# Kernel optimization log

Measured on AMD Instinct MI355X. Metric: run time of the kernel, lower is better.

The kernel has to match this reference:

```python
import jax, jax.numpy as jnp
import numpy as np
from jax import lax

SINKHORN_ITERS = 20
SINKHORN_REG = 0.05
OT_BLUR = 0.05
OT_ITERS = 20
LAMBDA_OT = 0.1
LAMBDA_REG = 0.01
N_SUB = 2048


def pairwise_dist_sq(a, b):
    # a: [B,N,3], b: [B,M,3] -> [B,N,M]
    a_sq = jnp.sum(a * a, axis=-1, keepdims=True)          # [B,N,1]
    b_sq = jnp.sum(b * b, axis=-1, keepdims=True)          # [B,M,1]
    ab = jnp.einsum('bnd,bmd->bnm', a, b)
    return jnp.maximum(a_sq + jnp.swapaxes(b_sq, 1, 2) - 2.0 * ab, 0.0)


def farthest_point_sample(x, n_sub):
    # x: [B,N,3] -> int32 indices [B,n_sub]; sequential min-distance update loop
    B, N, _ = x.shape

    def body(i, state):
        dists, farthest, sel = state
        sel = sel.at[:, i].set(farthest)
        centroid = jnp.take_along_axis(x, farthest[:, None, None], axis=1)  # [B,1,3]
        d = jnp.sum((x - centroid) ** 2, axis=-1)                            # [B,N]
        dists = jnp.minimum(dists, d)
        farthest = jnp.argmax(dists, axis=-1).astype(jnp.int32)
        return dists, farthest, sel

    dists = jnp.full((B, N), jnp.inf, dtype=x.dtype)
    farthest = jnp.zeros((B,), dtype=jnp.int32)
    sel = jnp.zeros((B, n_sub), dtype=jnp.int32)
    _, _, sel = lax.fori_loop(0, n_sub, body, (dists, farthest, sel))
    return sel


def sinkhorn_assignment(cost, n_iters=SINKHORN_ITERS, reg=SINKHORN_REG):
    # log-domain Sinkhorn -> soft doubly-stochastic P [B,N,M]
    log_K = -cost / reg
    B, N, M = cost.shape
    log_u = jnp.zeros((B, N), dtype=cost.dtype)
    log_v = jnp.zeros((B, M), dtype=cost.dtype)

    def body(carry, _):
        lu, lv = carry
        lu = -jax.nn.logsumexp(log_K + lv[:, None, :], axis=2)
        lv = -jax.nn.logsumexp(log_K + lu[:, :, None], axis=1)
        return (lu, lv), None

    (log_u, log_v), _ = lax.scan(body, (log_u, log_v), None, length=n_iters)
    return jnp.exp(log_K + log_u[:, :, None] + log_v[:, None, :])


def _ot_eps(x, y, eps, n_iters=OT_ITERS):
    # balanced entropic OT dual value per batch (geomloss sinkhorn, p=2: C=|x-y|^2/2)
    C = 0.5 * pairwise_dist_sq(x, y)
    B, N, M = C.shape
    log_mu = -jnp.log(jnp.asarray(N, C.dtype))
    log_nu = -jnp.log(jnp.asarray(M, C.dtype))
    f = jnp.zeros((B, N), dtype=C.dtype)
    g = jnp.zeros((B, M), dtype=C.dtype)

    def body(carry, _):
        f, g = carry
        f = -eps * jax.nn.logsumexp((g[:, None, :] - C) / eps + log_nu, axis=2)
        g = -eps * jax.nn.logsumexp((f[:, :, None] - C) / eps + log_mu, axis=1)
        return (f, g), None

    (f, g), _ = lax.scan(body, (f, g), None, length=n_iters)
    return jnp.mean(f, axis=1) + jnp.mean(g, axis=1)  # [B]


def sinkhorn_divergence(x, y, eps):
    return jnp.mean(_ot_eps(x, y, eps) - 0.5 * _ot_eps(x, x, eps) - 0.5 * _ot_eps(y, y, eps))


def _forward(target_sub, idx_dummy, t, template, W_enc, b_enc, W1, b1, W2, b2):
    pass


def setup_inputs() -> dict:
    key = jax.random.key(0)
    ks = jax.random.split(key, 9)
    B, N = 8, 16384
    d_z, d_h = 256, 256
    return {
        'target': jax.random.normal(ks[0], (B, N, 3), dtype=jnp.float32),
        't': jax.random.uniform(ks[1], (B,), dtype=jnp.float32),
        'template': jax.random.normal(ks[2], (N_SUB, 3), dtype=jnp.float32),
        'W_enc': jax.random.normal(ks[3], (3, d_z), dtype=jnp.float32) * 0.05,
        'b_enc': jnp.zeros((d_z,), dtype=jnp.float32),
        'W1': jax.random.normal(ks[4], (3 + 1 + d_z, d_h), dtype=jnp.float32) * 0.05,
        'b1': jnp.zeros((d_h,), dtype=jnp.float32),
        'W2': jax.random.normal(ks[5], (d_h, 3), dtype=jnp.float32) * 0.05,
        'b2': jnp.zeros((3,), dtype=jnp.float32),
    }


def reference(target, t, template, W_enc, b_enc, W1, b1, W2, b2):
    B, N, _ = target.shape
    n_sub = template.shape[0]
    t = jnp.clip(t, 1e-5, 1.0 - 1e-5)

    # FPS subsample target (n_sub < N); template already at n_sub points
    idx = farthest_point_sample(target, n_sub)                        # [B,n_sub]
    target_sub = jnp.take_along_axis(target, idx[:, :, None], axis=1)  # [B,n_sub,3]
    template_sub = jnp.broadcast_to(template[None], (B, n_sub, 3))

    # Sinkhorn OT alignment
    cost = pairwise_dist_sq(template_sub, target_sub)                  # [B,n_sub,n_sub]
    P = sinkhorn_assignment(cost)
    target_perm = jnp.einsum('bnm,bmd->bnd', P, target_sub)

    # straight-line interpolant + gt velocity
    v_gt = target_perm - template_sub
    t_ = t[:, None, None]
    x_t = (1.0 - t_) * template_sub + t_ * target_perm

    # encode (stand-in model): per-point linear + max-pool
    feat = jax.nn.relu(target_sub @ W_enc + b_enc)                     # [B,n_sub,d_z]
    z = jnp.max(feat, axis=1)                                          # [B,d_z]

    # velocity prediction (stand-in MLP conditioned on x_t, t, z)
    h_in = jnp.concatenate([
        x_t,
        jnp.broadcast_to(t_, (B, n_sub, 1)),
        jnp.broadcast_to(z[:, None, :], (B, n_sub, z.shape[-1])),
    ], axis=-1)
    v_pred = jax.nn.relu(h_in @ W1 + b1) @ W2 + b2                      # [B,n_sub,3]

    loss_velocity = jnp.mean((v_pred - v_gt) ** 2)

    # OT loss on x1 approx (no grad through v_pred, matching torch.no_grad)
    x_1_approx = template_sub + lax.stop_gradient(v_pred)
    eps = jnp.asarray(OT_BLUR ** 2, target.dtype)
    loss_ot = sinkhorn_divergence(x_1_approx, target_sub, eps)

    # template regularisation towards unit norm
    template_norms = jnp.sqrt(jnp.sum(template * template, axis=-1))
    loss_reg = jnp.mean((template_norms - 1.0) ** 2)

    loss = loss_velocity + LAMBDA_OT * loss_ot + LAMBDA_REG * loss_reg
    return loss, loss_velocity, loss_ot, loss_reg
```

## Files before the change

### kernel.cpp

```cpp
#include <hip/hip_runtime.h>
#include <math.h>

#define NPTS 16384
#define NB 8
#define NS 2048
#define DZ 256

typedef float v2f __attribute__((ext_vector_type(2)));

#define OFF_SCAL 0
#define OFF_LU   64
#define OFF_LV   (OFF_LU + NB*NS)
#define OFF_F    (OFF_LV + NB*NS)
#define OFF_G    (OFF_F + 3*NB*NS)
#define ZERO_FLOATS (OFF_G + 3*NB*NS)
#define OFF_IDX  ZERO_FLOATS
#define OFF_YP   (OFF_IDX + NB*NS)
#define OFF_TP   (OFF_YP + NB*NS*4)
#define OFF_XP   (OFF_TP + NS*4)
#define OFF_PERM (OFF_XP + NB*NS*4)
#define OFF_Z    (OFF_PERM + NB*NS*3)
#define OFF_HB   (OFF_Z + NB*DZ)

__global__ __launch_bounds__(512) void fps_kernel(const float* __restrict__ x,
                                                  int* __restrict__ sel){
  #pragma clang fp contract(off)
  const int b = blockIdx.x, tid = threadIdx.x;
  const float* xb = x + (size_t)b * NPTS * 3;
  float c[96];
  {
    const float4* s4 = (const float4*)(xb + (size_t)tid * 96);
    #pragma unroll
    for (int q = 0; q < 24; q++){
      float4 v = s4[q];
      c[4*q] = v.x; c[4*q+1] = v.y; c[4*q+2] = v.z; c[4*q+3] = v.w;
    }
  }
  v2f X[16], Y[16], Z[16], D[16];
  #pragma unroll
  for (int j = 0; j < 16; j++){
    X[j] = (v2f){c[6*j],   c[6*j+3]};
    Y[j] = (v2f){c[6*j+1], c[6*j+4]};
    Z[j] = (v2f){c[6*j+2], c[6*j+5]};
    D[j] = (v2f){INFINITY, INFINITY};
  }
  __shared__ unsigned long long sK[2][8];
  float c0 = xb[0], c1 = xb[1], c2 = xb[2];
  int widx = 0;
  const int wv = tid >> 6, lane = tid & 63;

  for (int i = 0; i < NS; i++){
    if (tid == 0) sel[b*NS + i] = widx;
    const v2f c0v = {c0,c0}, c1v = {c1,c1}, c2v = {c2,c2};
    #pragma unroll
    for (int j = 0; j < 16; j++){
      v2f dx = X[j] - c0v;
      v2f dy = Y[j] - c1v;
      v2f dz = Z[j] - c2v;
      v2f d2 = (dx*dx + dy*dy) + dz*dz;
      D[j] = __builtin_elementwise_min(D[j], d2);
    }
    v2f m0 = __builtin_elementwise_max(D[0],  D[1]);
    v2f m1 = __builtin_elementwise_max(D[2],  D[3]);
    v2f m2 = __builtin_elementwise_max(D[4],  D[5]);
    v2f m3 = __builtin_elementwise_max(D[6],  D[7]);
    v2f m4 = __builtin_elementwise_max(D[8],  D[9]);
    v2f m5 = __builtin_elementwise_max(D[10], D[11]);
    v2f m6 = __builtin_elementwise_max(D[12], D[13]);
    v2f m7 = __builtin_elementwise_max(D[14], D[15]);
    m0 = __builtin_elementwise_max(m0, m1);
    m2 = __builtin_elementwise_max(m2, m3);
    m4 = __builtin_elementwise_max(m4, m5);
    m6 = __builtin_elementwise_max(m6, m7);
    m0 = __builtin_elementwise_max(m0, m2);
    m4 = __builtin_elementwise_max(m4, m6);
    m0 = __builtin_elementwise_max(m0, m4);
    const float lmax = fmaxf(m0.x, m0.y);
    int kk = 31;
    #pragma unroll
    for (int j = 15; j >= 0; j--){
      if (D[j].y == lmax) kk = 2*j + 1;
      if (D[j].x == lmax) kk = 2*j;
    }
    unsigned long long key =
      ((unsigned long long)(~__float_as_uint(lmax)) << 32) |
      (unsigned int)(tid*32 + kk);
    #pragma unroll
    for (int o = 32; o; o >>= 1){
      unsigned long long ok = __shfl_xor(key, o, 64);
      key = (ok < key) ? ok : key;
    }
    const int par = i & 1;
    if (lane == 0) sK[par][wv] = key;
    __syncthreads();
    unsigned long long best = sK[par][0];
    #pragma unroll
    for (int w = 1; w < 8; w++){
      unsigned long long k2 = sK[par][w];
      best = (k2 < best) ? k2 : best;
    }
    widx = (int)(best & 0xffffffffu);
    const float* cp = xb + (size_t)widx * 3;
    c0 = cp[0]; c1 = cp[1]; c2 = cp[2];
  }
}

__global__ __launch_bounds__(256) void gather_pack_kernel(const float* __restrict__ x,
                                                          const int* __restrict__ sel,
                                                          float4* __restrict__ yp){
  const int b = blockIdx.y;
  const int k = blockIdx.x*256 + threadIdx.x;
  const int p = sel[b*NS + k];
  const float* s = x + ((size_t)b*NPTS + p)*3;
  const float x0 = s[0], x1 = s[1], x2 = s[2];
  const float sq = fmaf(x0,x0, fmaf(x1,x1, x2*x2));
  yp[b*NS + k] = make_float4(x0, x1, x2, sq);
}

__global__ __launch_bounds__(256) void pack_t_kernel(const float* __restrict__ tmpl,
                                                     float4* __restrict__ tp,
                                                     float* __restrict__ sumreg){
  __shared__ float sbuf[4];
  const int k = blockIdx.x*256 + threadIdx.x;
  const float x0 = tmpl[3*k], x1 = tmpl[3*k+1], x2 = tmpl[3*k+2];
  const float sq = fmaf(x0,x0, fmaf(x1,x1, x2*x2));
  tp[k] = make_float4(x0, x1, x2, sq);
  const float n = sqrtf(sq) - 1.0f;
  float v = n*n;
  #pragma unroll
  for (int o = 32; o; o >>= 1) v += __shfl_xor(v, o, 64);
  if ((threadIdx.x & 63) == 0) sbuf[threadIdx.x >> 6] = v;
  __syncthreads();
  if (threadIdx.x == 0){
    float t = 0.f;
    for (int w = 0; w < 4; w++) t += sbuf[w];
    atomicAdd(sumreg, t);
  }
}

__global__ __launch_bounds__(256) void feat_z_kernel(const float4* __restrict__ yp,
                                                     const float* __restrict__ Wenc,
                                                     const float* __restrict__ benc,
                                                     float* __restrict__ z){
  __shared__ float4 sy[NS];
  const int b = blockIdx.x, tid = threadIdx.x;
  for (int j = tid; j < NS; j += 256) sy[j] = yp[b*NS + j];
  __syncthreads();
  const float w0 = Wenc[tid], w1 = Wenc[256+tid], w2 = Wenc[512+tid], bb = benc[tid];
  float m = -INFINITY;
  for (int n = 0; n < NS; n++){
    float4 q = sy[n];
    float v = fmaf(q.x, w0, fmaf(q.y, w1, fmaf(q.z, w2, bb)));
    m = fmaxf(m, fmaxf(v, 0.0f));
  }
  z[b*DZ + tid] = m;
}

__global__ __launch_bounds__(256) void hbase_kernel(const float* __restrict__ z,
                                                    const float* __restrict__ W1,
                                                    const float* __restrict__ b1,
                                                    const float* __restrict__ tarr,
                                                    float* __restrict__ hb){
  __shared__ float sz[DZ];
  const int b = blockIdx.x, cidx = threadIdx.x;
  sz[cidx] = z[b*DZ + cidx];
  __syncthreads();
  const float t = fminf(fmaxf(tarr[b], 1e-5f), (float)(1.0 - 1e-5));
  float acc = fmaf(t, W1[3*256 + cidx], b1[cidx]);
  for (int k = 0; k < DZ; k++) acc = fmaf(sz[k], W1[(4 + k)*256 + cidx], acc);
  hb[b*DZ + cidx] = acc;
}

__device__ __forceinline__ void sink_pass_core(const float4* __restrict__ PI, long piStride,
                                               const float4* __restrict__ PJ, long pjStride,
                                               const float* __restrict__ dIn,
                                               float* __restrict__ dOut,
                                               float H, float twoH, float dMul, float dAdd,
                                               float oScale, float4* S){
  const int tid = threadIdx.x;
  const int b = blockIdx.z;
  {
    const float4* pj = PJ + pjStride*b;
    const float* din = dIn + (size_t)b*NS;
    for (int j = tid; j < NS; j += 1024){
      float4 q = pj[j];
      float E = fmaf(-H, q.w, fmaf(din[j], dMul, dAdd));
      S[j] = make_float4(q.x, q.y, q.z, E);
    }
  }
  __syncthreads();
  const int w = tid >> 6, lane = tid & 63;
  const int i = blockIdx.x*16 + w;
  const float4 pi = PI[piStride*b + i];
  const float R = -H*pi.w;
  float mx = -INFINITY, s = 0.0f;
  #pragma unroll 2
  for (int k = 0; k < 8; k++){
    const int j0 = k*256 + lane;
    float4 a0 = S[j0], a1 = S[j0+64], a2 = S[j0+128], a3 = S[j0+192];
    float v0 = fmaf(twoH, fmaf(pi.x,a0.x, fmaf(pi.y,a0.y, pi.z*a0.z)), a0.w + R);
    float v1 = fmaf(twoH, fmaf(pi.x,a1.x, fmaf(pi.y,a1.y, pi.z*a1.z)), a1.w + R);
    float v2 = fmaf(twoH, fmaf(pi.x,a2.x, fmaf(pi.y,a2.y, pi.z*a2.z)), a2.w + R);
    float v3 = fmaf(twoH, fmaf(pi.x,a3.x, fmaf(pi.y,a3.y, pi.z*a3.z)), a3.w + R);
    float m4 = fmaxf(fmaxf(v0, v1), fmaxf(v2, v3));
    float nm = fmaxf(mx, m4);
    s = fmaf(s, __expf(mx - nm),
             __expf(v0 - nm) + __expf(v1 - nm) + __expf(v2 - nm) + __expf(v3 - nm));
    mx = nm;
  }
  #pragma unroll
  for (int o = 32; o; o >>= 1){
    float om = __shfl_xor(mx, o, 64);
    float os = __shfl_xor(s,  o, 64);
    float nm = fmaxf(mx, om);
    s = fmaf(s, __expf(mx - nm), os*__expf(om - nm));
    mx = nm;
  }
  if (lane == 0) dOut[(size_t)b*NS + i] = oScale*(mx + __logf(s));
}

__global__ __launch_bounds__(1024) void sink_assign_kernel(const float4* __restrict__ tp,
                                                           const float4* __restrict__ yp,
                                                           float* __restrict__ lu,
                                                           float* __restrict__ lv,
                                                           int dir, float H, float twoH){
  __shared__ float4 S[NS];
  if (dir == 0) sink_pass_core(tp, 0,  yp, NS, lv, lu, H, twoH, 1.0f, 0.0f, -1.0f, S);
  else          sink_pass_core(yp, NS, tp, 0,  lu, lv, H, twoH, 1.0f, 0.0f, -1.0f, S);
}

__global__ __launch_bounds__(1024) void sink_ot_kernel(const float4* __restrict__ xp,
                                                       const float4* __restrict__ yp,
                                                       float* __restrict__ F,
                                                       float* __restrict__ G,
                                                       int dir, float H, float twoH,
                                                       float dMul, float dAdd, float oScale){
  __shared__ float4 S[NS];
  const int p = blockIdx.y;
  const float4* first  = (p == 2) ? yp : xp;
  const float4* second = (p == 1) ? xp : yp;
  float* f = F + (size_t)p*NB*NS;
  float* g = G + (size_t)p*NB*NS;
  if (dir == 0) sink_pass_core(first,  NS, second, NS, g, f, H, twoH, dMul, dAdd, oScale, S);
  else          sink_pass_core(second, NS, first,  NS, f, g, H, twoH, dMul, dAdd, oScale, S);
}

__global__ __launch_bounds__(1024) void perm_kernel(const float4* __restrict__ tp,
                                                    const float4* __restrict__ yp,
                                                    const float* __restrict__ lu,
                                                    const float* __restrict__ lv,
                                                    float* __restrict__ perm,
                                                    float H, float twoH){
  __shared__ float4 S[NS];
  const int tid = threadIdx.x, b = blockIdx.z;
  for (int j = tid; j < NS; j += 1024){
    float4 q = yp[(size_t)b*NS + j];
    float E = fmaf(-H, q.w, lv[(size_t)b*NS + j]);
    S[j] = make_float4(q.x, q.y, q.z, E);
  }
  __syncthreads();
  const int w = tid >> 6, lane = tid & 63;
  const int i = blockIdx.x*16 + w;
  const float4 pi = tp[i];
  const float R = fmaf(-H, pi.w, lu[(size_t)b*NS + i]);
  float a0 = 0.f, a1 = 0.f, a2 = 0.f;
  #pragma unroll 2
  for (int k = 0; k < 8; k++){
    #pragma unroll
    for (int u = 0; u < 4; u++){
      const int j = k*256 + u*64 + lane;
      float4 q = S[j];
      float val = fmaf(twoH, fmaf(pi.x,q.x, fmaf(pi.y,q.y, pi.z*q.z)), q.w + R);
      float wgt = __expf(val);
      a0 = fmaf(wgt, q.x, a0);
      a1 = fmaf(wgt, q.y, a1);
      a2 = fmaf(wgt, q.z, a2);
    }
  }
  #pragma unroll
  for (int o = 32; o; o >>= 1){
    a0 += __shfl_xor(a0, o, 64);
    a1 += __shfl_xor(a1, o, 64);
    a2 += __shfl_xor(a2, o, 64);
  }
  if (lane == 0){
    float* d = perm + ((size_t)b*NS + i)*3;
    d[0] = a0; d[1] = a1; d[2] = a2;
  }
}

__global__ __launch_bounds__(128) void mlp_kernel(const float4* __restrict__ tp,
                                                  const float* __restrict__ perm,
                                                  const float* __restrict__ hb,
                                                  const float* __restrict__ W1,
                                                  const float* __restrict__ W2,
                                                  const float* __restrict__ b2,
                                                  const float* __restrict__ tarr,
                                                  float4* __restrict__ xp,
                                                  float* __restrict__ sumvel){
  __shared__ float sw0[256], sw1[256], sw2[256], shb[256], sW2[768];
  __shared__ float sred[2];
  const int tid = threadIdx.x;
  const int r = blockIdx.x*128 + tid;
  const int b = r >> 11, n = r & (NS - 1);
  for (int k = tid; k < 256; k += 128){
    sw0[k] = W1[k]; sw1[k] = W1[256+k]; sw2[k] = W1[512+k]; shb[k] = hb[b*256 + k];
  }
  for (int k = tid; k < 768; k += 128) sW2[k] = W2[k];
  __syncthreads();
  const float t = fminf(fmaxf(tarr[b], 1e-5f), (float)(1.0 - 1e-5));
  const float4 T = tp[n];
  const float pm0 = perm[(size_t)r*3], pm1 = perm[(size_t)r*3+1], pm2 = perm[(size_t)r*3+2];
  const float omt = 1.0f - t;
  const float xt0 = omt*T.x + t*pm0;
  const float xt1 = omt*T.y + t*pm1;
  const float xt2 = omt*T.z + t*pm2;
  float a0 = b2[0], a1 = b2[1], a2 = b2[2];
  for (int cc = 0; cc < 256; cc++){
    float pre = fmaf(xt0, sw0[cc], fmaf(xt1, sw1[cc], fmaf(xt2, sw2[cc], shb[cc])));
    float h = fmaxf(pre, 0.0f);
    a0 = fmaf(h, sW2[3*cc],   a0);
    a1 = fmaf(h, sW2[3*cc+1], a1);
    a2 = fmaf(h, sW2[3*cc+2], a2);
  }
  const float vg0 = pm0 - T.x, vg1 = pm1 - T.y, vg2 = pm2 - T.z;
  const float d0 = a0 - vg0, d1 = a1 - vg1, d2 = a2 - vg2;
  float ls = fmaf(d0,d0, fmaf(d1,d1, d2*d2));
  const float x0 = T.x + a0, x1 = T.y + a1, x2 = T.z + a2;
  const float sq = fmaf(x0,x0, fmaf(x1,x1, x2*x2));
  xp[r] = make_float4(x0, x1, x2, sq);
  #pragma unroll
  for (int o = 32; o; o >>= 1) ls += __shfl_xor(ls, o, 64);
  if ((tid & 63) == 0) sred[tid >> 6] = ls;
  __syncthreads();
  if (tid == 0) atomicAdd(sumvel, sred[0] + sred[1]);
}

__global__ __launch_bounds__(256) void ot_sum_kernel(const float* __restrict__ F,
                                                     const float* __restrict__ G,
                                                     float* __restrict__ ot){
  __shared__ float sbuf[8];
  const int pb = blockIdx.x;
  const float* f = F + (size_t)pb*NS;
  const float* g = G + (size_t)pb*NS;
  float sf = 0.f, sg = 0.f;
  for (int j = threadIdx.x; j < NS; j += 256){ sf += f[j]; sg += g[j]; }
  #pragma unroll
  for (int o = 32; o; o >>= 1){ sf += __shfl_xor(sf, o, 64); sg += __shfl_xor(sg, o, 64); }
  if ((threadIdx.x & 63) == 0){ sbuf[threadIdx.x >> 6] = sf; sbuf[4 + (threadIdx.x >> 6)] = sg; }
  __syncthreads();
  if (threadIdx.x == 0){
    float tf = 0.f, tg = 0.f;
    for (int w = 0; w < 4; w++){ tf += sbuf[w]; tg += sbuf[4 + w]; }
    ot[pb] = tf/(float)NS + tg/(float)NS;
  }
}

__global__ void finalize_kernel(const float* __restrict__ scal, float* __restrict__ out){
  if (threadIdx.x == 0){
    const float* ot = scal + 2;
    float lot = 0.f;
    for (int b = 0; b < NB; b++)
      lot += ot[0*NB + b] - 0.5f*ot[1*NB + b] - 0.5f*ot[2*NB + b];
    lot /= (float)NB;
    const float lvv = scal[0] / (float)(NB*NS*3);
    const float lrg = scal[1] / (float)NS;
    out[0] = lvv + 0.1f*lot + 0.01f*lrg;
    out[1] = lvv;
    out[2] = lot;
    out[3] = lrg;
  }
}

extern "C" void kernel_launch(void* const* d_in, const int* in_sizes, int n_in,
                              void* d_out, int out_size, void* d_ws, size_t ws_size,
                              hipStream_t stream){
  (void)in_sizes; (void)n_in; (void)out_size; (void)ws_size;
  const float* target = (const float*)d_in[0];
  const float* tarr   = (const float*)d_in[1];
  const float* tmpl   = (const float*)d_in[2];
  const float* Wenc   = (const float*)d_in[3];
  const float* benc   = (const float*)d_in[4];
  const float* W1     = (const float*)d_in[5];
  const float* b1     = (const float*)d_in[6];
  const float* W2     = (const float*)d_in[7];
  const float* b2     = (const float*)d_in[8];
  float* out = (float*)d_out;
  float* ws  = (float*)d_ws;

  float*  scal = ws + OFF_SCAL;
  float*  lu   = ws + OFF_LU;
  float*  lv   = ws + OFF_LV;
  float*  F    = ws + OFF_F;
  float*  G    = ws + OFF_G;
  int*    sel  = (int*)(ws + OFF_IDX);
  float4* yp   = (float4*)(ws + OFF_YP);
  float4* tp   = (float4*)(ws + OFF_TP);
  float4* xp   = (float4*)(ws + OFF_XP);
  float*  perm = ws + OFF_PERM;
  float*  z    = ws + OFF_Z;
  float*  hb   = ws + OFF_HB;

  hipMemsetAsync(ws, 0, (size_t)ZERO_FLOATS*sizeof(float), stream);

  fps_kernel<<<NB, 512, 0, stream>>>(target, sel);
  gather_pack_kernel<<<dim3(8, NB), 256, 0, stream>>>(target, sel, yp);
  pack_t_kernel<<<8, 256, 0, stream>>>(tmpl, tp, scal + 1);
  feat_z_kernel<<<NB, 256, 0, stream>>>(yp, Wenc, benc, z);
  hbase_kernel<<<NB, 256, 0, stream>>>(z, W1, b1, tarr, hb);

  const float INVREG = 1.0f/0.05f;
  for (int it = 0; it < 20; ++it){
    sink_assign_kernel<<<dim3(128,1,NB), 1024, 0, stream>>>(tp, yp, lu, lv, 0, INVREG, 2.0f*INVREG);
    sink_assign_kernel<<<dim3(128,1,NB), 1024, 0, stream>>>(tp, yp, lu, lv, 1, INVREG, 2.0f*INVREG);
  }
  perm_kernel<<<dim3(128,1,NB), 1024, 0, stream>>>(tp, yp, lu, lv, perm, INVREG, 2.0f*INVREG);
  mlp_kernel<<<128, 128, 0, stream>>>(tp, perm, hb, W1, W2, b2, tarr, xp, scal + 0);

  const float EPS    = (float)(0.05*0.05);
  const float INVEPS = 1.0f/EPS;
  const float HOT    = 0.5f*INVEPS;
  const float LOGNU  = (float)(-log(2048.0));
  for (int it = 0; it < 20; ++it){
    sink_ot_kernel<<<dim3(128,3,NB), 1024, 0, stream>>>(xp, yp, F, G, 0, HOT, INVEPS, INVEPS, LOGNU, -EPS);
    sink_ot_kernel<<<dim3(128,3,NB), 1024, 0, stream>>>(xp, yp, F, G, 1, HOT, INVEPS, INVEPS, LOGNU, -EPS);
  }
  ot_sum_kernel<<<24, 256, 0, stream>>>(F, G, scal + 2);
  finalize_kernel<<<1, 64, 0, stream>>>(scal, out);
}
```

Baseline: 5.748 ms.

## Restructure FPS argmax reduction: float-max shuffle, ballot, and winner-thread broadcast

The per-iteration argmax in farthest point sampling now reduces a plain float max with shuffles and picks the first matching lane by ballot, instead of shuffling 64-bit keys. Only the winning thread locates its local index and writes the centroid coordinates to shared memory, so the dependent global load of the next centroid is removed. This adds a second __syncthreads per iteration and drops the double-buffered key array. Launch bounds now request two blocks per CU.

```diff
diff --git a/kernel.cpp b/kernel.cpp
--- a/kernel.cpp
+++ b/kernel.cpp
@@ -22,8 +22,8 @@
 #define OFF_Z    (OFF_PERM + NB*NS*3)
 #define OFF_HB   (OFF_Z + NB*DZ)
 
-__global__ __launch_bounds__(512) void fps_kernel(const float* __restrict__ x,
-                                                  int* __restrict__ sel){
+__global__ __launch_bounds__(512, 2) void fps_kernel(const float* __restrict__ x,
+                                                     int* __restrict__ sel){
   #pragma clang fp contract(off)
   const int b = blockIdx.x, tid = threadIdx.x;
   const float* xb = x + (size_t)b * NPTS * 3;
@@ -44,7 +44,9 @@
     Z[j] = (v2f){c[6*j+2], c[6*j+5]};
     D[j] = (v2f){INFINITY, INFINITY};
   }
-  __shared__ unsigned long long sK[2][8];
+  __shared__ unsigned long long sK[8];
+  __shared__ float sC[3];
+  __shared__ int sW;
   float c0 = xb[0], c1 = xb[1], c2 = xb[2];
   int widx = 0;
   const int wv = tid >> 6, lane = tid & 63;
@@ -76,32 +78,37 @@
     m4 = __builtin_elementwise_max(m4, m6);
     m0 = __builtin_elementwise_max(m0, m4);
     const float lmax = fmaxf(m0.x, m0.y);
-    int kk = 31;
+    float wmax = lmax;
     #pragma unroll
-    for (int j = 15; j >= 0; j--){
-      if (D[j].y == lmax) kk = 2*j + 1;
-      if (D[j].x == lmax) kk = 2*j;
-    }
-    unsigned long long key =
-      ((unsigned long long)(~__float_as_uint(lmax)) << 32) |
-      (unsigned int)(tid*32 + kk);
-    #pragma unroll
-    for (int o = 32; o; o >>= 1){
-      unsigned long long ok = __shfl_xor(key, o, 64);
-      key = (ok < key) ? ok : key;
-    }
-    const int par = i & 1;
-    if (lane == 0) sK[par][wv] = key;
+    for (int o = 32; o; o >>= 1) wmax = fmaxf(wmax, __shfl_xor(wmax, o, 64));
+    const unsigned long long bal = __ballot(lmax == wmax);
+    if (lane == 0){
+      const int ftid = wv*64 + (__ffsll(bal) - 1);
+      sK[wv] = ((unsigned long long)(~__float_as_uint(wmax)) << 32) | (unsigned)ftid;
+    }
     __syncthreads();
-    unsigned long long best = sK[par][0];
+    unsigned long long best = sK[0];
     #pragma unroll
     for (int w = 1; w < 8; w++){
-      unsigned long long k2 = sK[par][w];
+      unsigned long long k2 = sK[w];
       best = (k2 < best) ? k2 : best;
     }
-    widx = (int)(best & 0xffffffffu);
-    const float* cp = xb + (size_t)widx * 3;
-    c0 = cp[0]; c1 = cp[1]; c2 = cp[2];
+    const int wtid = (int)(best & 0xffffffffu);
+    if (tid == wtid){
+      const float bmax = __uint_as_float(~(unsigned)(best >> 32));
+      int kk = 31;
+      float px = 0.f, py = 0.f, pz = 0.f;
+      #pragma unroll
+      for (int j = 15; j >= 0; j--){
+        if (D[j].y == bmax){ kk = 2*j + 1; px = X[j].y; py = Y[j].y; pz = Z[j].y; }
+        if (D[j].x == bmax){ kk = 2*j;     px = X[j].x; py = Y[j].x; pz = Z[j].x; }
+      }
+      sW = tid*32 + kk;
+      sC[0] = px; sC[1] = py; sC[2] = pz;
+    }
+    __syncthreads();
+    widx = sW;
+    c0 = sC[0]; c1 = sC[1]; c2 = sC[2];
   }
 }
 
```

After: 5.933 ms. 1.03x slower.

## Restructure FPS argmax with DPP wave max, ballot, and shared centroid broadcast

Applied to the files above, without the earlier changes.

Restructures the per-iteration argmax in the farthest point sampling loop. The running max is folded into the distance update, a DPP-based wave max replaces the 64-bit key shuffle reduction, and ballot picks the first winning lane. Only that lane computes the index and writes the centroid coordinates to shared memory. This drops the dependent global load of the new centroid from the serial loop, shortening the critical path per iteration, at the cost of extra shared traffic and a launch-bounds occupancy hint.

```diff
diff --git a/kernel.cpp b/kernel.cpp
--- a/kernel.cpp
+++ b/kernel.cpp
@@ -22,8 +22,25 @@
 #define OFF_Z    (OFF_PERM + NB*NS*3)
 #define OFF_HB   (OFF_Z + NB*DZ)
 
-__global__ __launch_bounds__(512) void fps_kernel(const float* __restrict__ x,
-                                                  int* __restrict__ sel){
+__device__ __forceinline__ float wave_max_dpp(float v){
+  int t;
+  t = __builtin_amdgcn_update_dpp(__float_as_int(v), __float_as_int(v), 0x111, 0xf, 0xf, false);
+  v = fmaxf(v, __int_as_float(t));
+  t = __builtin_amdgcn_update_dpp(__float_as_int(v), __float_as_int(v), 0x112, 0xf, 0xf, false);
+  v = fmaxf(v, __int_as_float(t));
+  t = __builtin_amdgcn_update_dpp(__float_as_int(v), __float_as_int(v), 0x114, 0xf, 0xf, false);
+  v = fmaxf(v, __int_as_float(t));
+  t = __builtin_amdgcn_update_dpp(__float_as_int(v), __float_as_int(v), 0x118, 0xf, 0xf, false);
+  v = fmaxf(v, __int_as_float(t));
+  t = __builtin_amdgcn_update_dpp(__float_as_int(v), __float_as_int(v), 0x142, 0xa, 0xf, false);
+  v = fmaxf(v, __int_as_float(t));
+  t = __builtin_amdgcn_update_dpp(__float_as_int(v), __float_as_int(v), 0x143, 0xc, 0xf, false);
+  v = fmaxf(v, __int_as_float(t));
+  return __shfl(v, 63, 64);
+}
+
+__global__ __launch_bounds__(512, 2) void fps_kernel(const float* __restrict__ x,
+                                                     int* __restrict__ sel){
   #pragma clang fp contract(off)
   const int b = blockIdx.x, tid = threadIdx.x;
   const float* xb = x + (size_t)b * NPTS * 3;
@@ -45,63 +62,54 @@
     D[j] = (v2f){INFINITY, INFINITY};
   }
   __shared__ unsigned long long sK[2][8];
+  __shared__ float4 sC[2][8];
   float c0 = xb[0], c1 = xb[1], c2 = xb[2];
   int widx = 0;
   const int wv = tid >> 6, lane = tid & 63;
 
   for (int i = 0; i < NS; i++){
     if (tid == 0) sel[b*NS + i] = widx;
-    const v2f c0v = {c0,c0}, c1v = {c1,c1}, c2v = {c2,c2};
+    const float n0 = -c0, n1 = -c1, n2 = -c2;
+    const v2f n0v = {n0,n0}, n1v = {n1,n1}, n2v = {n2,n2};
+    v2f lm = {0.0f, 0.0f};
     #pragma unroll
     for (int j = 0; j < 16; j++){
-      v2f dx = X[j] - c0v;
-      v2f dy = Y[j] - c1v;
-      v2f dz = Z[j] - c2v;
+      v2f dx = X[j] + n0v;
+      v2f dy = Y[j] + n1v;
+      v2f dz = Z[j] + n2v;
       v2f d2 = (dx*dx + dy*dy) + dz*dz;
-      D[j] = __builtin_elementwise_min(D[j], d2);
-    }
-    v2f m0 = __builtin_elementwise_max(D[0],  D[1]);
-    v2f m1 = __builtin_elementwise_max(D[2],  D[3]);
-    v2f m2 = __builtin_elementwise_max(D[4],  D[5]);
-    v2f m3 = __builtin_elementwise_max(D[6],  D[7]);
-    v2f m4 = __builtin_elementwise_max(D[8],  D[9]);
-    v2f m5 = __builtin_elementwise_max(D[10], D[11]);
-    v2f m6 = __builtin_elementwise_max(D[12], D[13]);
-    v2f m7 = __builtin_elementwise_max(D[14], D[15]);
-    m0 = __builtin_elementwise_max(m0, m1);
-    m2 = __builtin_elementwise_max(m2, m3);
-    m4 = __builtin_elementwise_max(m4, m5);
-    m6 = __builtin_elementwise_max(m6, m7);
-    m0 = __builtin_elementwise_max(m0, m2);
-    m4 = __builtin_elementwise_max(m4, m6);
-    m0 = __builtin_elementwise_max(m0, m4);
-    const float lmax = fmaxf(m0.x, m0.y);
-    int kk = 31;
-    #pragma unroll
-    for (int j = 15; j >= 0; j--){
-      if (D[j].y == lmax) kk = 2*j + 1;
-      if (D[j].x == lmax) kk = 2*j;
-    }
-    unsigned long long key =
-      ((unsigned long long)(~__float_as_uint(lmax)) << 32) |
-      (unsigned int)(tid*32 + kk);
-    #pragma unroll
-    for (int o = 32; o; o >>= 1){
-      unsigned long long ok = __shfl_xor(key, o, 64);
-      key = (ok < key) ? ok : key;
-    }
+      v2f nd = __builtin_elementwise_min(D[j], d2);
+      D[j] = nd;
+      lm = __builtin_elementwise_max(lm, nd);
+    }
+    const float lmax = fmaxf(lm.x, lm.y);
+    const float wmax = wave_max_dpp(lmax);
+    const unsigned long long bal = __ballot(lmax == wmax);
+    const int ftid = wv*64 + (__ffsll((long long)bal) - 1);
     const int par = i & 1;
-    if (lane == 0) sK[par][wv] = key;
+    if (tid == ftid){
+      int kk = 31;
+      float px = 0.f, py = 0.f, pz = 0.f;
+      #pragma unroll
+      for (int j = 15; j >= 0; j--){
+        if (D[j].y == wmax){ kk = 2*j + 1; px = X[j].y; py = Y[j].y; pz = Z[j].y; }
+        if (D[j].x == wmax){ kk = 2*j;     px = X[j].x; py = Y[j].x; pz = Z[j].x; }
+      }
+      sK[par][wv] = ((unsigned long long)(~__float_as_uint(wmax)) << 32) |
+                    (unsigned)(tid*32 + kk);
+      sC[par][wv] = make_float4(px, py, pz, 0.f);
+    }
     __syncthreads();
     unsigned long long best = sK[par][0];
+    int sidx = 0;
     #pragma unroll
     for (int w = 1; w < 8; w++){
       unsigned long long k2 = sK[par][w];
-      best = (k2 < best) ? k2 : best;
+      if (k2 < best){ best = k2; sidx = w; }
     }
     widx = (int)(best & 0xffffffffu);
-    const float* cp = xb + (size_t)widx * 3;
-    c0 = cp[0]; c1 = cp[1]; c2 = cp[2];
+    const float4 cc = sC[par][sidx];
+    c0 = cc.x; c1 = cc.y; c2 = cc.z;
   }
 }
 
```

Result: slower. 7.822 ms (+36.1%).

## Process four rows per wave in Sinkhorn passes to reuse shared tiles

Applied to the files above, without the earlier changes.

Each wavefront now computes the logsumexp for four output rows instead of one, reusing every shared-memory column load across the four rows. The grid is shrunk accordingly from 128 to 32 blocks per batch, which also cuts the redundant per-block staging of the column data into shared memory. The trade-offs are higher register pressure and fewer blocks, which lowers occupancy and latency hiding.

```diff
diff --git a/kernel.cpp b/kernel.cpp
--- a/kernel.cpp
+++ b/kernel.cpp
@@ -190,33 +190,46 @@
   }
   __syncthreads();
   const int w = tid >> 6, lane = tid & 63;
-  const int i = blockIdx.x*16 + w;
-  const float4 pi = PI[piStride*b + i];
-  const float R = -H*pi.w;
-  float mx = -INFINITY, s = 0.0f;
+  const int i0 = blockIdx.x*64 + w*4;
+  float4 pi[4];
+  float  R[4], mx[4], ss[4];
+  #pragma unroll
+  for (int r = 0; r < 4; r++){
+    pi[r] = PI[piStride*b + i0 + r];
+    R[r]  = -H*pi[r].w;
+    mx[r] = -INFINITY;
+    ss[r] = 0.0f;
+  }
   #pragma unroll 2
   for (int k = 0; k < 8; k++){
     const int j0 = k*256 + lane;
     float4 a0 = S[j0], a1 = S[j0+64], a2 = S[j0+128], a3 = S[j0+192];
-    float v0 = fmaf(twoH, fmaf(pi.x,a0.x, fmaf(pi.y,a0.y, pi.z*a0.z)), a0.w + R);
-    float v1 = fmaf(twoH, fmaf(pi.x,a1.x, fmaf(pi.y,a1.y, pi.z*a1.z)), a1.w + R);
-    float v2 = fmaf(twoH, fmaf(pi.x,a2.x, fmaf(pi.y,a2.y, pi.z*a2.z)), a2.w + R);
-    float v3 = fmaf(twoH, fmaf(pi.x,a3.x, fmaf(pi.y,a3.y, pi.z*a3.z)), a3.w + R);
-    float m4 = fmaxf(fmaxf(v0, v1), fmaxf(v2, v3));
-    float nm = fmaxf(mx, m4);
-    s = fmaf(s, __expf(mx - nm),
-             __expf(v0 - nm) + __expf(v1 - nm) + __expf(v2 - nm) + __expf(v3 - nm));
-    mx = nm;
-  }
-  #pragma unroll
-  for (int o = 32; o; o >>= 1){
-    float om = __shfl_xor(mx, o, 64);
-    float os = __shfl_xor(s,  o, 64);
-    float nm = fmaxf(mx, om);
-    s = fmaf(s, __expf(mx - nm), os*__expf(om - nm));
-    mx = nm;
-  }
-  if (lane == 0) dOut[(size_t)b*NS + i] = oScale*(mx + __logf(s));
+    #pragma unroll
+    for (int r = 0; r < 4; r++){
+      float v0 = fmaf(twoH, fmaf(pi[r].x,a0.x, fmaf(pi[r].y,a0.y, pi[r].z*a0.z)), a0.w + R[r]);
+      float v1 = fmaf(twoH, fmaf(pi[r].x,a1.x, fmaf(pi[r].y,a1.y, pi[r].z*a1.z)), a1.w + R[r]);
+      float v2 = fmaf(twoH, fmaf(pi[r].x,a2.x, fmaf(pi[r].y,a2.y, pi[r].z*a2.z)), a2.w + R[r]);
+      float v3 = fmaf(twoH, fmaf(pi[r].x,a3.x, fmaf(pi[r].y,a3.y, pi[r].z*a3.z)), a3.w + R[r]);
+      float m4 = fmaxf(fmaxf(v0, v1), fmaxf(v2, v3));
+      float nm = fmaxf(mx[r], m4);
+      ss[r] = fmaf(ss[r], __expf(mx[r] - nm),
+                   __expf(v0 - nm) + __expf(v1 - nm) + __expf(v2 - nm) + __expf(v3 - nm));
+      mx[r] = nm;
+    }
+  }
+  #pragma unroll
+  for (int r = 0; r < 4; r++){
+    float m = mx[r], s = ss[r];
+    #pragma unroll
+    for (int o = 32; o; o >>= 1){
+      float om = __shfl_xor(m, o, 64);
+      float os = __shfl_xor(s, o, 64);
+      float nm = fmaxf(m, om);
+      s = fmaf(s, __expf(m - nm), os*__expf(om - nm));
+      m = nm;
+    }
+    if (lane == 0) dOut[(size_t)b*NS + i0 + r] = oScale*(m + __logf(s));
+  }
 }
 
 __global__ __launch_bounds__(1024) void sink_assign_kernel(const float4* __restrict__ tp,
@@ -411,8 +424,8 @@
 
   const float INVREG = 1.0f/0.05f;
   for (int it = 0; it < 20; ++it){
-    sink_assign_kernel<<<dim3(128,1,NB), 1024, 0, stream>>>(tp, yp, lu, lv, 0, INVREG, 2.0f*INVREG);
-    sink_assign_kernel<<<dim3(128,1,NB), 1024, 0, stream>>>(tp, yp, lu, lv, 1, INVREG, 2.0f*INVREG);
+    sink_assign_kernel<<<dim3(32,1,NB), 1024, 0, stream>>>(tp, yp, lu, lv, 0, INVREG, 2.0f*INVREG);
+    sink_assign_kernel<<<dim3(32,1,NB), 1024, 0, stream>>>(tp, yp, lu, lv, 1, INVREG, 2.0f*INVREG);
   }
   perm_kernel<<<dim3(128,1,NB), 1024, 0, stream>>>(tp, yp, lu, lv, perm, INVREG, 2.0f*INVREG);
   mlp_kernel<<<128, 128, 0, stream>>>(tp, perm, hb, W1, W2, b2, tarr, xp, scal + 0);
@@ -422,8 +435,8 @@
   const float HOT    = 0.5f*INVEPS;
   const float LOGNU  = (float)(-log(2048.0));
   for (int it = 0; it < 20; ++it){
-    sink_ot_kernel<<<dim3(128,3,NB), 1024, 0, stream>>>(xp, yp, F, G, 0, HOT, INVEPS, INVEPS, LOGNU, -EPS);
-    sink_ot_kernel<<<dim3(128,3,NB), 1024, 0, stream>>>(xp, yp, F, G, 1, HOT, INVEPS, INVEPS, LOGNU, -EPS);
+    sink_ot_kernel<<<dim3(32,3,NB), 1024, 0, stream>>>(xp, yp, F, G, 0, HOT, INVEPS, INVEPS, LOGNU, -EPS);
+    sink_ot_kernel<<<dim3(32,3,NB), 1024, 0, stream>>>(xp, yp, F, G, 1, HOT, INVEPS, INVEPS, LOGNU, -EPS);
   }
   ot_sum_kernel<<<24, 256, 0, stream>>>(F, G, scal + 2);
   finalize_kernel<<<1, 64, 0, stream>>>(scal, out);
```

After: 5.792 ms. About the same (+0.8%).
